# Performance work log

Measured on AMD Instinct MI355X. Metric: run time of the kernel, lower is better.

The kernel has to match this reference:

```python
import jax, jax.numpy as jnp
import numpy as np
import math

NP_, NA_ = 100000, 50000          # paper / author node counts
E0, E1, E2 = 300000, 300000, 200000  # author->paper, paper->author, paper->paper
H, D = 4, 16
HID = H * D                       # 64
IN_DIM, OUT_DIM = 128, 64
L = 2                             # num_layers
EPS = 1e-5


def _lin(x, W, b):
    return x @ W + b


def _ln(x, g, b):
    m = jnp.mean(x, axis=-1, keepdims=True)
    v = jnp.mean((x - m) ** 2, axis=-1, keepdims=True)
    return (x - m) * jax.lax.rsqrt(v + EPS) * g + b


def _segment_softmax(a, seg, n):
    m = jax.ops.segment_max(a, seg, num_segments=n)
    a = jnp.exp(a - m[seg])
    s = jax.ops.segment_sum(a, seg, num_segments=n)
    return a / (s[seg] + 1e-16)


def _hgt_conv(h_p, h_a, ei_ap, ei_pa, ei_pp,
              W_kqv, b_kqv, W_krel, W_vrel, p_rel, W_hout, b_hout, skip):
    # per-node-type fused KQV projection (HeteroDictLinear)
    kqv_p = _lin(h_p, W_kqv[0], b_kqv[0])   # [NP, 3*HID]
    kqv_a = _lin(h_a, W_kqv[1], b_kqv[1])   # [NA, 3*HID]
    k_p, q_p, v_p = [t.reshape(-1, H, D) for t in jnp.split(kqv_p, 3, axis=1)]
    k_a, q_a, v_a = [t.reshape(-1, H, D) for t in jnp.split(kqv_a, 3, axis=1)]
    # destination (query) concat order: paper then author -> dst offsets {paper:0, author:NP}
    Q = jnp.concatenate([q_p, q_a], axis=0)                    # [NP+NA, H, D]
    # per-(edge_type, head) DxD relation transforms on source k/v (k_rel / v_rel)
    # src concat order follows edge types: et0 src=author, et1 src=paper, et2 src=paper
    Ks = jnp.concatenate([
        jnp.einsum('nhd,hde->nhe', k_a, W_krel[0]),
        jnp.einsum('nhd,hde->nhe', k_p, W_krel[1]),
        jnp.einsum('nhd,hde->nhe', k_p, W_krel[2]),
    ], axis=0)                                                 # [NA+2*NP, H, D]
    Vs = jnp.concatenate([
        jnp.einsum('nhd,hde->nhe', v_a, W_vrel[0]),
        jnp.einsum('nhd,hde->nhe', v_p, W_vrel[1]),
        jnp.einsum('nhd,hde->nhe', v_p, W_vrel[2]),
    ], axis=0)
    # bipartite global edge index (src offsets: 0, NA, NA+NP; dst offsets: paper 0, author NP)
    src = jnp.concatenate([ei_ap[0], ei_pa[0] + NA_, ei_pp[0] + NA_ + NP_])
    dst = jnp.concatenate([ei_ap[1], ei_pa[1] + NP_, ei_pp[1]])
    p = jnp.concatenate([
        jnp.broadcast_to(p_rel[0], (E0, H)),
        jnp.broadcast_to(p_rel[1], (E1, H)),
        jnp.broadcast_to(p_rel[2], (E2, H)),
    ], axis=0)                                                 # [E, H]
    # edge-wise attention: alpha = (q_i * k_j).sum(-1) * p_rel / sqrt(D), segment-softmax over dst
    alpha = jnp.einsum('ehd,ehd->eh', Q[dst], Ks[src]) * p / math.sqrt(D)
    alpha = _segment_softmax(alpha, dst, NP_ + NA_)
    out = jax.ops.segment_sum(Vs[src] * alpha[:, :, None], dst,
                              num_segments=NP_ + NA_)          # [NP+NA, H, D]
    out = out.reshape(-1, HID)
    g = jax.nn.gelu(out, approximate=False)
    o_p = _lin(g[:NP_], W_hout[0], b_hout[0])
    o_a = _lin(g[NP_:], W_hout[1], b_hout[1])
    a_p = jax.nn.sigmoid(skip[0])
    a_a = jax.nn.sigmoid(skip[1])
    return a_p * o_p + (1.0 - a_p) * h_p, a_a * o_a + (1.0 - a_a) * h_a


def _forward(x_paper, x_author, ei_ap, ei_pa, ei_pp,
             W_in, b_in, W_kqv, b_kqv, W_krel, W_vrel, p_rel,
             W_hout, b_hout, skip, ln_g, ln_b, W_out, b_out):
    h_p = _lin(x_paper, W_in[0], b_in[0])
    h_a = _lin(x_author, W_in[1], b_in[1])
    for l in range(L):
        h_p, h_a = _hgt_conv(h_p, h_a, ei_ap, ei_pa, ei_pp,
                             W_kqv[l], b_kqv[l], W_krel[l], W_vrel[l],
                             p_rel[l], W_hout[l], b_hout[l], skip[l])
        h_p = jax.nn.gelu(_ln(h_p, ln_g[l, 0], ln_b[l, 0]), approximate=False)
        h_a = jax.nn.gelu(_ln(h_a, ln_g[l, 1], ln_b[l, 1]), approximate=False)
        # dropout is identity at eval
    out_p = _lin(h_p, W_out[0], b_out[0])
    out_a = _lin(h_a, W_out[1], b_out[1])
    return jnp.concatenate([out_p, out_a], axis=0)  # [NP+NA, OUT_DIM]


def setup_inputs() -> dict:
    key = jax.random.key(0)
    ks = jax.random.split(key, 20)
    f32 = jnp.float32

    def nrm(k, shape, fan_in):
        return jax.random.normal(k, shape, dtype=f32) * (1.0 / math.sqrt(fan_in))

    inp = {}
    inp['x_paper'] = jax.random.normal(ks[0], (NP_, IN_DIM), dtype=f32)
    inp['x_author'] = jax.random.normal(ks[1], (NA_, IN_DIM), dtype=f32)
    inp['ei_ap'] = jnp.stack([jax.random.randint(ks[2], (E0,), 0, NA_),
                              jax.random.randint(ks[3], (E0,), 0, NP_)]).astype(jnp.int32)
    inp['ei_pa'] = jnp.stack([jax.random.randint(ks[4], (E1,), 0, NP_),
                              jax.random.randint(ks[5], (E1,), 0, NA_)]).astype(jnp.int32)
    inp['ei_pp'] = jnp.stack([jax.random.randint(ks[6], (E2,), 0, NP_),
                              jax.random.randint(ks[7], (E2,), 0, NP_)]).astype(jnp.int32)
    inp['W_in'] = nrm(ks[8], (2, IN_DIM, HID), IN_DIM)
    inp['b_in'] = jnp.zeros((2, HID), f32)
    inp['W_kqv'] = nrm(ks[9], (L, 2, HID, 3 * HID), HID)
    inp['b_kqv'] = jnp.zeros((L, 2, 3 * HID), f32)
    inp['W_krel'] = nrm(ks[10], (L, 3, H, D, D), D)
    inp['W_vrel'] = nrm(ks[11], (L, 3, H, D, D), D)
    inp['p_rel'] = jnp.ones((L, 3, H), f32)
    inp['W_hout'] = nrm(ks[12], (L, 2, HID, HID), HID)
    inp['b_hout'] = jnp.zeros((L, 2, HID), f32)
    inp['skip'] = jnp.ones((L, 2), f32)
    inp['ln_g'] = jnp.ones((L, 2, HID), f32)
    inp['ln_b'] = jnp.zeros((L, 2, HID), f32)
    inp['W_out'] = nrm(ks[13], (2, HID, OUT_DIM), HID)
    inp['b_out'] = jnp.zeros((2, OUT_DIM), f32)
    return inp


def reference(x_paper, x_author, ei_ap, ei_pa, ei_pp,
              W_in, b_in, W_kqv, b_kqv, W_krel, W_vrel, p_rel,
              W_hout, b_hout, skip, ln_g, ln_b, W_out, b_out):
    return _forward(x_paper, x_author, ei_ap, ei_pa, ei_pp,
                    W_in, b_in, W_kqv, b_kqv, W_krel, W_vrel, p_rel,
                    W_hout, b_hout, skip, ln_g, ln_b, W_out, b_out)
```

## Files before the change

kernel.cpp:

```cpp
#include <hip/hip_runtime.h>
#include <hip/hip_bf16.h>

#define NP 100000
#define NA 50000
#define NTOT 150000
#define E0 300000
#define E1 300000
#define E2 200000
#define ETOT 800000
#define NH 4
#define HD 16
#define HID 64
#define IN_DIM 128
#define KQV 192
#define LAYERS 2
#define NSRC 250000
#define JP 320
#define JA 192
#define NCH 586
#define PT 1563
#define AT 782
#define LSPAN 33280

typedef __attribute__((ext_vector_type(8))) short bf16x8;
typedef __attribute__((ext_vector_type(4))) float f32x4;
typedef _Float16 h16x2 __attribute__((ext_vector_type(2)));

__device__ __forceinline__ float gelu_exact(float x) {
    return 0.5f * x * (1.0f + erff(x * 0.7071067811865475f));
}
__device__ __forceinline__ unsigned short f2bf(float f) {
    unsigned u = __float_as_uint(f);
    return (unsigned short)((u + 0x7fffu + ((u >> 16) & 1u)) >> 16);
}
__device__ __forceinline__ float bf2f(unsigned short b) {
    return __uint_as_float((unsigned)b << 16);
}
__device__ __forceinline__ unsigned short f2h(float f) {
    union { _Float16 h; unsigned short u; } c;
    c.h = (_Float16)f;
    return c.u;
}

__device__ __forceinline__ void edge_decode(int e, const int* __restrict__ ei_ap,
                                            const int* __restrict__ ei_pa,
                                            const int* __restrict__ ei_pp,
                                            int& src, int& dst) {
    if (e < E0)            { src = ei_ap[e];                 dst = ei_ap[E0 + e]; }
    else if (e < E0 + E1)  { int le = e - E0;
                             src = NA + ei_pa[le];           dst = NP + ei_pa[E1 + le]; }
    else                   { int le = e - E0 - E1;
                             src = NA + NP + ei_pp[le];      dst = ei_pp[E2 + le]; }
}

__global__ void csr_count_kernel(const int* __restrict__ ei_ap, const int* __restrict__ ei_pa,
                                 const int* __restrict__ ei_pp, int* __restrict__ cnt) {
    int e = blockIdx.x * 256 + threadIdx.x;
    if (e >= ETOT) return;
    int src, dst; edge_decode(e, ei_ap, ei_pa, ei_pp, src, dst);
    atomicAdd(&cnt[dst], 1);
}

__global__ void scan_chunk_sums(const int* __restrict__ cnt, int* __restrict__ csum) {
    __shared__ int sd[256];
    int c = blockIdx.x, t = threadIdx.x;
    int i = c * 256 + t;
    sd[t] = (i < NTOT) ? cnt[i] : 0;
    __syncthreads();
    for (int o = 128; o > 0; o >>= 1) { if (t < o) sd[t] += sd[t + o]; __syncthreads(); }
    if (t == 0) csum[c] = sd[0];
}

__global__ void scan_offsets(const int* __restrict__ csum, int* __restrict__ coff, int nch) {
    __shared__ int sd[1024];
    int t = threadIdx.x;
    int v = (t < nch) ? csum[t] : 0;
    sd[t] = v;
    __syncthreads();
    for (int o = 1; o < 1024; o <<= 1) {
        int x = (t >= o) ? sd[t - o] : 0;
        __syncthreads();
        sd[t] += x;
        __syncthreads();
    }
    if (t < nch) coff[t] = sd[t] - v;
}

__global__ void scan_final(const int* __restrict__ cnt, const int* __restrict__ coff,
                           int* __restrict__ row_ptr, int* __restrict__ cursor) {
    __shared__ int sd[256];
    int c = blockIdx.x, t = threadIdx.x, i = c * 256 + t;
    int v = (i < NTOT) ? cnt[i] : 0;
    sd[t] = v;
    __syncthreads();
    for (int o = 1; o < 256; o <<= 1) {
        int x = (t >= o) ? sd[t - o] : 0;
        __syncthreads();
        sd[t] += x;
        __syncthreads();
    }
    if (i < NTOT) { int ex = coff[c] + sd[t] - v; row_ptr[i] = ex; cursor[i] = ex; }
    if (i == 0) row_ptr[NTOT] = ETOT;
}

__global__ void csr_fill_kernel(const int* __restrict__ ei_ap, const int* __restrict__ ei_pa,
                                const int* __restrict__ ei_pp, int* __restrict__ cursor,
                                int* __restrict__ edge_src) {
    int e = blockIdx.x * 256 + threadIdx.x;
    if (e >= ETOT) return;
    int src, dst; edge_decode(e, ei_ap, ei_pa, ei_pp, src, dst);
    int pos = atomicAdd(&cursor[dst], 1);
    edge_src[pos] = src;
}

__global__ void prep_weights(const float* __restrict__ W_in, const float* __restrict__ W_hout,
                             const float* __restrict__ W_out,
                             unsigned short* __restrict__ WinT,
                             unsigned short* __restrict__ WhoutT,
                             unsigned short* __restrict__ WoutT) {
    int idx = blockIdx.x * 256 + threadIdx.x;
    if (idx < 2 * 64 * IN_DIM) {
        int t = idx >> 13, r = idx & 8191;
        int c = r >> 7, k = r & 127;
        WinT[idx] = f2bf(W_in[(size_t)t * IN_DIM * HID + (size_t)k * HID + c]);
        return;
    }
    int i2 = idx - 2 * 64 * IN_DIM;
    if (i2 < LAYERS * 2 * 4096) {
        int p = i2 >> 12, r = i2 & 4095;
        int c = r >> 6, k = r & 63;
        WhoutT[i2] = f2bf(W_hout[(size_t)p * 4096 + (size_t)k * HID + c]);
        return;
    }
    int i3 = i2 - LAYERS * 2 * 4096;
    if (i3 < 2 * 4096) {
        int p = i3 >> 12, r = i3 & 4095;
        int c = r >> 6, k = r & 63;
        WoutT[i3] = f2bf(W_out[(size_t)p * 4096 + (size_t)k * HID + c]);
    }
}

__global__ void fuse_weights_all(const float* __restrict__ Wkqv, const float* __restrict__ bkqv,
                                 const float* __restrict__ Wkrel, const float* __restrict__ Wvrel,
                                 unsigned short* __restrict__ WfpT, float* __restrict__ bfp,
                                 unsigned short* __restrict__ WfaT, float* __restrict__ bfa) {
    int gidx = blockIdx.x * 256 + threadIdx.x;
    if (gidx >= LAYERS * LSPAN) return;
    int lay = gidx / LSPAN;
    int idx = gidx - lay * LSPAN;
    const float* Wkqv_l = Wkqv + (size_t)lay * 2 * HID * KQV;
    const float* bkqv_l = bkqv + (size_t)lay * 2 * KQV;
    const float* Wkrel_l = Wkrel + (size_t)lay * 3 * NH * HD * HD;
    const float* Wvrel_l = Wvrel + (size_t)lay * 3 * NH * HD * HD;
    unsigned short* WfpT_l = WfpT + (size_t)lay * JP * 64;
    unsigned short* WfaT_l = WfaT + (size_t)lay * JA * 64;
    float* bfp_l = bfp + (size_t)lay * JP;
    float* bfa_l = bfa + (size_t)lay * JA;

    int type, i, j;
    if (idx < 65 * JP) { type = 0; i = idx / JP; j = idx % JP; }
    else {
        int r = idx - 65 * JP;
        type = 1; i = r / JA; j = r % JA;
    }
    int c = j >> 6, jj = j & 63, h = jj >> 4, e = jj & 15;
    const float* Wk = Wkqv_l + (size_t)type * HID * KQV;
    const float* bk = bkqv_l + type * KQV;
    float val;
    if (c == 0) {
        val = (i < 64) ? Wk[i * KQV + 64 + jj] : bk[64 + jj];
    } else {
        int et, isV;
        if (type == 0) { et = (c == 1 || c == 3) ? 1 : 2; isV = (c >= 3); }
        else           { et = 0; isV = (c == 2); }
        const float* Wr = (isV ? Wvrel_l : Wkrel_l) + (size_t)(et * NH + h) * HD * HD;
        int sb = (isV ? 128 : 0) + h * HD;
        val = 0.0f;
        #pragma unroll
        for (int d = 0; d < HD; d++) {
            float a = (i < 64) ? Wk[i * KQV + sb + d] : bk[sb + d];
            val += a * Wr[d * HD + e];
        }
    }
    if (i < 64) (type ? WfaT_l : WfpT_l)[(size_t)j * 64 + i] = f2bf(val);
    else        (type ? bfa_l : bfp_l)[j] = val;
}

__device__ __forceinline__ void mfma64(const unsigned short* A, const unsigned short* W,
                                       int wr, int wc, int lrow, int lgrp,
                                       f32x4& a00, f32x4& a01, f32x4& a10, f32x4& a11) {
    a00 = (f32x4){0.f,0.f,0.f,0.f}; a01 = a00; a10 = a00; a11 = a00;
    #pragma unroll
    for (int ks = 0; ks < 2; ks++) {
        int ko = ks * 32 + lgrp * 8;
        bf16x8 x0 = *(const bf16x8*)&A[(wr + lrow) * 72 + ko];
        bf16x8 x1 = *(const bf16x8*)&A[(wr + 16 + lrow) * 72 + ko];
        bf16x8 w0 = *(const bf16x8*)&W[(wc + lrow) * 72 + ko];
        bf16x8 w1 = *(const bf16x8*)&W[(wc + 16 + lrow) * 72 + ko];
        a00 = __builtin_amdgcn_mfma_f32_16x16x32_bf16(x0, w0, a00, 0, 0, 0);
        a01 = __builtin_amdgcn_mfma_f32_16x16x32_bf16(x0, w1, a01, 0, 0, 0);
        a10 = __builtin_amdgcn_mfma_f32_16x16x32_bf16(x1, w0, a10, 0, 0, 0);
        a11 = __builtin_amdgcn_mfma_f32_16x16x32_bf16(x1, w1, a11, 0, 0, 0);
    }
}

__device__ __forceinline__ void store_q(f32x4 a00, f32x4 a01, f32x4 a10, f32x4 a11,
                                        float bq0, float bq1, int c0, int c1, bool even,
                                        int nb, int N, int wr, int lgrp,
                                        unsigned short* Qbase) {
    #pragma unroll
    for (int mi = 0; mi < 2; mi++) {
        const f32x4 a0 = mi ? a10 : a00;
        const f32x4 a1 = mi ? a11 : a01;
        int rbase = wr + mi * 16 + lgrp * 4;
        #pragma unroll
        for (int r = 0; r < 4; r++) {
            int n = nb + rbase + r;
            unsigned own = (unsigned)f2h(a0[r] + bq0) | ((unsigned)f2h(a1[r] + bq1) << 16);
            unsigned oth = __shfl_xor(own, 1, 64);
            if (even && n < N) {
                unsigned* qp = (unsigned*)(Qbase + (size_t)n * HID);
                qp[c0 >> 1] = (own & 0xffffu) | (oth << 16);
                qp[c1 >> 1] = (own >> 16) | (oth & 0xffff0000u);
            }
        }
    }
}

__device__ __forceinline__ void store_kv(f32x4 k00, f32x4 k01, f32x4 k10, f32x4 k11,
                                         f32x4 v00, f32x4 v01, f32x4 v10, f32x4 v11,
                                         float bk0, float bk1, float bv0, float bv1,
                                         int c0, int c1, bool even,
                                         int nb, int N, int wr, int lgrp,
                                         int noff, unsigned* KVb) {
    #pragma unroll
    for (int mi = 0; mi < 2; mi++) {
        const f32x4 ak0 = mi ? k10 : k00;
        const f32x4 ak1 = mi ? k11 : k01;
        const f32x4 av0 = mi ? v10 : v00;
        const f32x4 av1 = mi ? v11 : v01;
        int rbase = wr + mi * 16 + lgrp * 4;
        #pragma unroll
        for (int r = 0; r < 4; r++) {
            int n = nb + rbase + r;
            unsigned own0 = (unsigned)f2h(ak0[r] + bk0) | ((unsigned)f2h(av0[r] + bv0) << 16);
            unsigned oth0 = __shfl_xor(own0, 1, 64);
            unsigned own1 = (unsigned)f2h(ak1[r] + bk1) | ((unsigned)f2h(av1[r] + bv1) << 16);
            unsigned oth1 = __shfl_xor(own1, 1, 64);
            if (n < N) {
                unsigned* dst = KVb + (((size_t)(noff + n)) << 6);
                unsigned w0 = even ? ((own0 & 0xffffu) | (oth0 << 16))
                                   : ((oth0 >> 16) | (own0 & 0xffff0000u));
                unsigned w1 = even ? ((own1 & 0xffffu) | (oth1 << 16))
                                   : ((oth1 >> 16) | (own1 & 0xffff0000u));
                dst[c0] = w0;
                dst[c1] = w1;
            }
        }
    }
}

__device__ __forceinline__ void kqv_phase(const unsigned short* HS,
                                          unsigned short* PA, unsigned short* PB,
                                          const unsigned short* WT, const float* bias2,
                                          int type, int tid, int nb, int N,
                                          int wr, int wc, int lrow, int lgrp,
                                          int c0, int c1, bool even,
                                          unsigned short* Qh, unsigned* KVb) {
    #pragma unroll
    for (int it = 0; it < 4; it++) {
        int idx = it * 256 + tid;
        int c = idx >> 4, kg = (idx & 15) * 4;
        *(ushort4*)&PA[c * 72 + kg] = *(const ushort4*)(WT + (size_t)c * 64 + kg);
    }
    __syncthreads();
    {
        f32x4 q00, q01, q10, q11;
        mfma64(HS, PA, wr, wc, lrow, lgrp, q00, q01, q10, q11);
        store_q(q00, q01, q10, q11, bias2[c0], bias2[c1], c0, c1, even,
                nb, N, wr, lgrp, Qh + (size_t)(type ? NP : 0) * HID);
    }
    __syncthreads();
    int ng = type ? 1 : 2;
    for (int g = 0; g < ng; g++) {
        int kc = type ? 64 : (g ? 128 : 64);
        int vc = type ? 128 : (g ? 256 : 192);
        int nf = type ? 0 : (g ? NA + NP : NA);
        #pragma unroll
        for (int it = 0; it < 4; it++) {
            int idx = it * 256 + tid;
            int c = idx >> 4, kg = (idx & 15) * 4;
            *(ushort4*)&PA[c * 72 + kg] = *(const ushort4*)(WT + (size_t)(kc + c) * 64 + kg);
            *(ushort4*)&PB[c * 72 + kg] = *(const ushort4*)(WT + (size_t)(vc + c) * 64 + kg);
        }
        __syncthreads();
        f32x4 k00, k01, k10, k11, v00, v01, v10, v11;
        mfma64(HS, PA, wr, wc, lrow, lgrp, k00, k01, k10, k11);
        mfma64(HS, PB, wr, wc, lrow, lgrp, v00, v01, v10, v11);
        store_kv(k00, k01, k10, k11, v00, v01, v10, v11,
                 bias2[kc + c0], bias2[kc + c1], bias2[vc + c0], bias2[vc + c1],
                 c0, c1, even, nb, N, wr, lgrp, nf, KVb);
        __syncthreads();
    }
}

__device__ __forceinline__ void mfma_r16(const unsigned short* X, const unsigned short* P,
                                         int w16, int lrow, int lgrp, f32x4* acc) {
    #pragma unroll
    for (int f = 0; f < 4; f++) acc[f] = (f32x4){0.f, 0.f, 0.f, 0.f};
    #pragma unroll
    for (int ks = 0; ks < 2; ks++) {
        int ko = ks * 32 + lgrp * 8;
        bf16x8 a = *(const bf16x8*)&X[(w16 + lrow) * 72 + ko];
        #pragma unroll
        for (int f = 0; f < 4; f++) {
            bf16x8 bb = *(const bf16x8*)&P[(f * 16 + lrow) * 72 + ko];
            acc[f] = __builtin_amdgcn_mfma_f32_16x16x32_bf16(a, bb, acc[f], 0, 0, 0);
        }
    }
}

__device__ __forceinline__ void store_q4(const f32x4* q, const float* bias,
                                         int lrow, int lgrp, int w16, int nb, int N,
                                         bool even, unsigned short* Qbase) {
    #pragma unroll
    for (int fp = 0; fp < 4; fp += 2) {
        int c0 = fp * 16 + lrow, c1 = c0 + 16;
        float b0 = bias[c0], b1 = bias[c1];
        #pragma unroll
        for (int r = 0; r < 4; r++) {
            int n = nb + w16 + lgrp * 4 + r;
            unsigned own = (unsigned)f2h(q[fp][r] + b0) | ((unsigned)f2h(q[fp + 1][r] + b1) << 16);
            unsigned oth = __shfl_xor(own, 1, 64);
            if (even && n < N) {
                unsigned* qp = (unsigned*)(Qbase + (size_t)n * HID);
                qp[c0 >> 1] = (own & 0xffffu) | (oth << 16);
                qp[c1 >> 1] = (own >> 16) | (oth & 0xffff0000u);
            }
        }
    }
}

__device__ __forceinline__ void store_kv4(const f32x4* kk, const f32x4* vv,
                                          const float* bias, int kc, int vc,
                                          int lrow, int lgrp, int w16, int nb, int N,
                                          bool even, int noff, unsigned* KVb) {
    #pragma unroll
    for (int fp = 0; fp < 4; fp += 2) {
        int c0 = fp * 16 + lrow, c1 = c0 + 16;
        float bk0 = bias[kc + c0], bk1 = bias[kc + c1];
        float bv0 = bias[vc + c0], bv1 = bias[vc + c1];
        #pragma unroll
        for (int r = 0; r < 4; r++) {
            int n = nb + w16 + lgrp * 4 + r;
            unsigned own0 = (unsigned)f2h(kk[fp][r] + bk0) | ((unsigned)f2h(vv[fp][r] + bv0) << 16);
            unsigned oth0 = __shfl_xor(own0, 1, 64);
            unsigned own1 = (unsigned)f2h(kk[fp + 1][r] + bk1) | ((unsigned)f2h(vv[fp + 1][r] + bv1) << 16);
            unsigned oth1 = __shfl_xor(own1, 1, 64);
            if (n < N) {
                unsigned* dst = KVb + (((size_t)(noff + n)) << 6);
                unsigned w0 = even ? ((own0 & 0xffffu) | (oth0 << 16))
                                   : ((oth0 >> 16) | (own0 & 0xffff0000u));
                unsigned w1 = even ? ((own1 & 0xffffu) | (oth1 << 16))
                                   : ((oth1 >> 16) | (own1 & 0xffff0000u));
                dst[c0] = w0;
                dst[c1] = w1;
            }
        }
    }
}

#define STAGE_PANEL(dst, src)                                                   \
    { _Pragma("unroll")                                                         \
      for (int it_ = 0; it_ < 4; it_++) {                                       \
          int idx_ = it_ * 256 + tid;                                           \
          int c_ = idx_ >> 4, kg_ = (idx_ & 15) * 4;                            \
          *(ushort4*)&dst[c_ * 72 + kg_] =                                      \
              *(const ushort4*)((src) + (size_t)c_ * 64 + kg_);                 \
      } }

__global__ __launch_bounds__(256) void gemm_in_kqv(
    const float* __restrict__ xp, const float* __restrict__ xa,
    const unsigned short* __restrict__ WinT, const float* __restrict__ b_in,
    const unsigned short* __restrict__ WfpT, const float* __restrict__ bfp,
    const unsigned short* __restrict__ WfaT, const float* __restrict__ bfa,
    unsigned short* __restrict__ Hb, unsigned short* __restrict__ Qh,
    unsigned* __restrict__ KVb)
{
    __shared__ unsigned short smem[17408];
    unsigned short* XB  = smem;
    unsigned short* WTl = smem + 8704;
    unsigned short* HS  = smem;
    unsigned short* PA  = smem + 4608;
    unsigned short* PB  = smem + 9216;

    int b = blockIdx.x, tid = threadIdx.x;
    int type = (b >= PT);
    int tile = type ? (b - PT) : b;
    int N = type ? NA : NP;
    const float* X = type ? xa : xp;
    const unsigned short* WT = WinT + (size_t)type * 64 * IN_DIM;
    const float* bias = b_in + type * HID;
    unsigned short* H = Hb + (type ? (size_t)NP * HID : 0);
    int nb = tile * 64;

    {
        int row = tid >> 2, cg = (tid & 3) * 32;
        int n = nb + row;
        if (n < N) {
            const float* xr = X + (size_t)n * IN_DIM + cg;
            #pragma unroll
            for (int i = 0; i < 32; i += 4) {
                float4 v = *(const float4*)(xr + i);
                *(ushort4*)&XB[row * 136 + cg + i] =
                    make_ushort4(f2bf(v.x), f2bf(v.y), f2bf(v.z), f2bf(v.w));
            }
        } else {
            #pragma unroll
            for (int i = 0; i < 32; i += 4)
                *(ushort4*)&XB[row * 136 + cg + i] = make_ushort4(0, 0, 0, 0);
        }
    }
    #pragma unroll
    for (int it = 0; it < 8; it++) {
        int idx = it * 256 + tid;
        int c = idx >> 5, kg = (idx & 31) * 4;
        *(ushort4*)&WTl[c * 136 + kg] = *(const ushort4*)(WT + (size_t)c * IN_DIM + kg);
    }
    __syncthreads();

    int w = tid >> 6, lane = tid & 63;
    int wr = (w >> 1) * 32, wc = (w & 1) * 32;
    int lrow = lane & 15, lgrp = lane >> 4;
    int c0 = wc + lrow, c1 = wc + 16 + lrow;
    bool even = ((lrow & 1) == 0);

    f32x4 acc00 = {0.f,0.f,0.f,0.f}, acc01 = {0.f,0.f,0.f,0.f};
    f32x4 acc10 = {0.f,0.f,0.f,0.f}, acc11 = {0.f,0.f,0.f,0.f};
    #pragma unroll
    for (int ks = 0; ks < 4; ks++) {
        int ko = ks * 32 + lgrp * 8;
        bf16x8 a0 = *(const bf16x8*)&XB[(wr + lrow) * 136 + ko];
        bf16x8 a1 = *(const bf16x8*)&XB[(wr + 16 + lrow) * 136 + ko];
        bf16x8 b0 = *(const bf16x8*)&WTl[(wc + lrow) * 136 + ko];
        bf16x8 b1 = *(const bf16x8*)&WTl[(wc + 16 + lrow) * 136 + ko];
        acc00 = __builtin_amdgcn_mfma_f32_16x16x32_bf16(a0, b0, acc00, 0, 0, 0);
        acc01 = __builtin_amdgcn_mfma_f32_16x16x32_bf16(a0, b1, acc01, 0, 0, 0);
        acc10 = __builtin_amdgcn_mfma_f32_16x16x32_bf16(a1, b0, acc10, 0, 0, 0);
        acc11 = __builtin_amdgcn_mfma_f32_16x16x32_bf16(a1, b1, acc11, 0, 0, 0);
    }
    __syncthreads();

    float bias0 = bias[c0], bias1 = bias[c1];
    #pragma unroll
    for (int mi = 0; mi < 2; mi++) {
        const f32x4 accn0 = mi ? acc10 : acc00;
        const f32x4 accn1 = mi ? acc11 : acc01;
        int rbase = wr + mi * 16 + lgrp * 4;
        #pragma unroll
        for (int r = 0; r < 4; r++) {
            int n = nb + rbase + r;
            unsigned short h0 = f2bf(accn0[r] + bias0);
            unsigned short h1 = f2bf(accn1[r] + bias1);
            HS[(rbase + r) * 72 + c0] = h0;
            HS[(rbase + r) * 72 + c1] = h1;
            unsigned own = (unsigned)h0 | ((unsigned)h1 << 16);
            unsigned oth = __shfl_xor(own, 1, 64);
            if (even && n < N) {
                unsigned* hp = (unsigned*)(H + (size_t)n * HID);
                hp[c0 >> 1] = (own & 0xffffu) | (oth << 16);
                hp[c1 >> 1] = (own >> 16) | (oth & 0xffff0000u);
            }
        }
    }
    __syncthreads();

    const unsigned short* WT2 = type ? WfaT : WfpT;
    const float* bias2 = type ? bfa : bfp;
    kqv_phase(HS, PA, PB, WT2, bias2, type, tid, nb, N,
              wr, wc, lrow, lgrp, c0, c1, even, Qh, KVb);
}

__global__ __launch_bounds__(256) void attn_kernel(
    const unsigned short* __restrict__ Qh, const unsigned* __restrict__ KVb,
    const float* __restrict__ p_rel, const int* __restrict__ row_ptr,
    const int* __restrict__ edge_src, unsigned short* __restrict__ ABf)
{
    int wid = threadIdx.x >> 6, lane = threadIdx.x & 63;
    int n = blockIdx.x * 4 + wid;
    if (n >= NTOT) return;
    int half = lane >> 5;
    int p = lane & 31;
    int h = p >> 3;
    unsigned qw = *(const unsigned*)(Qh + (((size_t)n) << 6) + 2 * p);
    union { unsigned u; h16x2 v; _Float16 f[2]; } qc; qc.u = qw;
    h16x2 qh = qc.v;
    const float INV_LN2 = 1.4426950408889634f;
    float pr0 = p_rel[h] * 0.25f * INV_LN2;
    float pr1 = p_rel[4 + h] * 0.25f * INV_LN2;
    float pr2 = p_rel[8 + h] * 0.25f * INV_LN2;
    int beg = row_ptr[n], end = row_ptr[n + 1];
    float s = 0.0f, acc0 = 0.f, acc1 = 0.f;
    for (int e = beg; e < end; e += 4) {
        int e0 = e + half;
        int e1 = e + 2 + half;
        bool v0 = (e0 < end), v1 = (e1 < end);
        int s0 = v0 ? edge_src[e0] : 0;
        int s1 = v1 ? edge_src[e1] : 0;
        uint2 kv0 = *(const uint2*)(KVb + (((size_t)s0) << 6) + 2 * p);
        uint2 kv1 = *(const uint2*)(KVb + (((size_t)s1) << 6) + 2 * p);
        float d0, d1;
#if __has_builtin(__builtin_amdgcn_fdot2)
        {
            union { unsigned u; h16x2 v; } ck;
            ck.u = kv0.x; d0 = __builtin_amdgcn_fdot2(qh, ck.v, 0.0f, false);
            ck.u = kv1.x; d1 = __builtin_amdgcn_fdot2(qh, ck.v, 0.0f, false);
        }
#else
        {
            union { unsigned u; _Float16 f[2]; } ck;
            float q0 = (float)qc.f[0], q1 = (float)qc.f[1];
            ck.u = kv0.x; d0 = q0 * (float)ck.f[0] + q1 * (float)ck.f[1];
            ck.u = kv1.x; d1 = q0 * (float)ck.f[0] + q1 * (float)ck.f[1];
        }
#endif
        d0 += __shfl_xor(d0, 1, 64);  d1 += __shfl_xor(d1, 1, 64);
        d0 += __shfl_xor(d0, 2, 64);  d1 += __shfl_xor(d1, 2, 64);
        d0 += __shfl_xor(d0, 4, 64);  d1 += __shfl_xor(d1, 4, 64);
        float pa = (s0 < NA) ? pr0 : ((s0 < NA + NP) ? pr1 : pr2);
        float pb = (s1 < NA) ? pr0 : ((s1 < NA + NP) ? pr1 : pr2);
        float a0 = v0 ? fminf(d0 * pa, 80.0f) : -INFINITY;
        float a1 = v1 ? fminf(d1 * pb, 80.0f) : -INFINITY;
        float p0 = exp2f(a0);
        float p1 = exp2f(a1);
        s += p0 + p1;
        union { unsigned u; _Float16 f[2]; } cv0, cv1;
        cv0.u = kv0.y; cv1.u = kv1.y;
        acc0 += p0 * (float)cv0.f[0] + p1 * (float)cv1.f[0];
        acc1 += p0 * (float)cv0.f[1] + p1 * (float)cv1.f[1];
    }
    s    += __shfl_xor(s, 32, 64);
    acc0 += __shfl_xor(acc0, 32, 64);
    acc1 += __shfl_xor(acc1, 32, 64);
    if (half == 0) {
        float inv = 1.0f / (s + 1e-16f);
        unsigned pack = (unsigned)f2bf(acc0 * inv) | ((unsigned)f2bf(acc1 * inv) << 16);
        *(unsigned*)(ABf + (((size_t)n) << 6) + 2 * p) = pack;
    }
}

__global__ __launch_bounds__(256) void gemm_hout_fused(
    const unsigned short* __restrict__ ABf, const unsigned short* __restrict__ WhT,
    const float* __restrict__ bhout, const float* __restrict__ skip_p,
    const float* __restrict__ lng, const float* __restrict__ lnb,
    unsigned short* __restrict__ Hb,
    const unsigned short* __restrict__ WfpT, const float* __restrict__ bfp,
    const unsigned short* __restrict__ WfaT, const float* __restrict__ bfa,
    unsigned short* __restrict__ Qh, unsigned* __restrict__ KVb,
    const unsigned short* __restrict__ WoT, const float* __restrict__ bout,
    float* __restrict__ outp)
{
    __shared__ unsigned short smem[13824];
    unsigned short* XbS = smem;
    unsigned short* PA  = smem + 4608;
    unsigned short* PB  = smem + 9216;

    int b = blockIdx.x, tid = threadIdx.x;
    int type = (b >= PT);
    int tile = type ? (b - PT) : b;
    int N = type ? NA : NP;
    size_t base_off = type ? (size_t)NP * HID : 0;
    const unsigned short* X = ABf + base_off;
    const unsigned short* W = WhT + (size_t)type * 4096;
    const float* bias = bhout + type * HID;
    unsigned short* H = Hb + base_off;
    int nb = tile * 64;
    bool fin = (WoT != nullptr);

    {
        int row = tid >> 2, cg = (tid & 3) * 16;
        int n = nb + row;
        unsigned short tmp[16];
        if (n < N) {
            const unsigned short* xr = X + (((size_t)n) << 6) + cg;
            #pragma unroll
            for (int i = 0; i < 16; i += 4) {
                ushort4 v = *(const ushort4*)(xr + i);
                tmp[i]   = f2bf(gelu_exact(bf2f(v.x)));
                tmp[i+1] = f2bf(gelu_exact(bf2f(v.y)));
                tmp[i+2] = f2bf(gelu_exact(bf2f(v.z)));
                tmp[i+3] = f2bf(gelu_exact(bf2f(v.w)));
            }
        } else {
            #pragma unroll
            for (int i = 0; i < 16; i++) tmp[i] = 0;
        }
        #pragma unroll
        for (int i = 0; i < 16; i += 4)
            *(ushort4*)&XbS[row * 72 + cg + i] =
                make_ushort4(tmp[i], tmp[i+1], tmp[i+2], tmp[i+3]);
    }
    STAGE_PANEL(PA, W)
    __syncthreads();

    int w = tid >> 6, lane = tid & 63;
    int lrow = lane & 15, lgrp = lane >> 4;
    int w16 = w * 16;
    bool even = ((lrow & 1) == 0);

    f32x4 acc[4];
    mfma_r16(XbS, PA, w16, lrow, lgrp, acc);
    const unsigned short* WT2 = type ? WfaT : WfpT;
    const float* bias2 = type ? bfa : bfp;
    STAGE_PANEL(PB, fin ? (WoT + (size_t)type * 4096) : WT2)

    float a = 1.0f / (1.0f + __expf(-skip_p[type]));
    float oma = 1.0f - a;
    float lnv[4][4];
    {
        float bh[4], gg[4], ll[4];
        #pragma unroll
        for (int f = 0; f < 4; f++) {
            int c = f * 16 + lrow;
            bh[f] = bias[c];
            gg[f] = lng[type * HID + c];
            ll[f] = lnb[type * HID + c];
        }
        #pragma unroll
        for (int r = 0; r < 4; r++) {
            int n = nb + w16 + lgrp * 4 + r;
            float x0, x1, x2, x3;
            if (n < N) {
                const unsigned short* hp = H + (size_t)n * HID;
                x0 = a * (acc[0][r] + bh[0]) + oma * bf2f(hp[0 * 16 + lrow]);
                x1 = a * (acc[1][r] + bh[1]) + oma * bf2f(hp[1 * 16 + lrow]);
                x2 = a * (acc[2][r] + bh[2]) + oma * bf2f(hp[2 * 16 + lrow]);
                x3 = a * (acc[3][r] + bh[3]) + oma * bf2f(hp[3 * 16 + lrow]);
            } else { x0 = x1 = x2 = x3 = 0.f; }
            float sum = x0 + x1 + x2 + x3;
            sum += __shfl_xor(sum, 1, 64); sum += __shfl_xor(sum, 2, 64);
            sum += __shfl_xor(sum, 4, 64); sum += __shfl_xor(sum, 8, 64);
            float mean = sum * (1.0f / 64.0f);
            float d0 = x0 - mean, d1 = x1 - mean, d2 = x2 - mean, d3 = x3 - mean;
            float sq = d0*d0 + d1*d1 + d2*d2 + d3*d3;
            sq += __shfl_xor(sq, 1, 64); sq += __shfl_xor(sq, 2, 64);
            sq += __shfl_xor(sq, 4, 64); sq += __shfl_xor(sq, 8, 64);
            float rstd = rsqrtf(sq * (1.0f / 64.0f) + 1e-5f);
            lnv[r][0] = gelu_exact(d0 * rstd * gg[0] + ll[0]);
            lnv[r][1] = gelu_exact(d1 * rstd * gg[1] + ll[1]);
            lnv[r][2] = gelu_exact(d2 * rstd * gg[2] + ll[2]);
            lnv[r][3] = gelu_exact(d3 * rstd * gg[3] + ll[3]);
            if (!fin && n < N) {
                #pragma unroll
                for (int fp = 0; fp < 4; fp += 2) {
                    int c0 = fp * 16 + lrow, c1 = c0 + 16;
                    unsigned own = (unsigned)f2bf(lnv[r][fp]) | ((unsigned)f2bf(lnv[r][fp + 1]) << 16);
                    unsigned oth = __shfl_xor(own, 1, 64);
                    if (even) {
                        unsigned* hp2 = (unsigned*)(H + (size_t)n * HID);
                        hp2[c0 >> 1] = (own & 0xffffu) | (oth << 16);
                        hp2[c1 >> 1] = (own >> 16) | (oth & 0xffff0000u);
                    }
                }
            } else if (!fin) {
                #pragma unroll
                for (int fp = 0; fp < 4; fp += 2) {
                    unsigned own = 0;
                    (void)__shfl_xor(own, 1, 64);
                }
            }
        }
    }
    __syncthreads();

    #pragma unroll
    for (int r = 0; r < 4; r++) {
        int row = w16 + lgrp * 4 + r;
        #pragma unroll
        for (int f = 0; f < 4; f++)
            XbS[row * 72 + f * 16 + lrow] = f2bf(lnv[r][f]);
    }
    __syncthreads();

    if (fin) {
        f32x4 o[4];
        mfma_r16(XbS, PB, w16, lrow, lgrp, o);
        const float* b2 = bout + type * HID;
        float* O = outp + base_off;
        #pragma unroll
        for (int f = 0; f < 4; f++) {
            int c = f * 16 + lrow;
            float bb = b2[c];
            #pragma unroll
            for (int r = 0; r < 4; r++) {
                int n = nb + w16 + lgrp * 4 + r;
                if (n < N) O[(size_t)n * HID + c] = o[f][r] + bb;
            }
        }
        return;
    }

    int kc1 = 64, vc1 = type ? 128 : 192;
    int nf1 = type ? 0 : NA;
    {
        f32x4 q[4];
        mfma_r16(XbS, PB, w16, lrow, lgrp, q);
        STAGE_PANEL(PA, WT2 + (size_t)kc1 * 64)
        store_q4(q, bias2, lrow, lgrp, w16, nb, N, even,
                 Qh + (size_t)(type ? NP : 0) * HID);
    }
    __syncthreads();

    f32x4 kk[4];
    mfma_r16(XbS, PA, w16, lrow, lgrp, kk);
    STAGE_PANEL(PB, WT2 + (size_t)vc1 * 64)
    __syncthreads();

    {
        f32x4 vv[4];
        mfma_r16(XbS, PB, w16, lrow, lgrp, vv);
        if (type == 0) STAGE_PANEL(PA, WT2 + (size_t)128 * 64)
        store_kv4(kk, vv, bias2, kc1, vc1, lrow, lgrp, w16, nb, N, even, nf1, KVb);
    }
    if (type == 0) {
        __syncthreads();
        mfma_r16(XbS, PA, w16, lrow, lgrp, kk);
        STAGE_PANEL(PB, WT2 + (size_t)256 * 64)
        __syncthreads();
        f32x4 vv[4];
        mfma_r16(XbS, PB, w16, lrow, lgrp, vv);
        store_kv4(kk, vv, bias2, 128, 256, lrow, lgrp, w16, nb, N, even, NA + NP, KVb);
    }
}

extern "C" void kernel_launch(void* const* d_in, const int* in_sizes, int n_in,
                              void* d_out, int out_size, void* d_ws, size_t ws_size,
                              hipStream_t stream) {
    const float* x_paper  = (const float*)d_in[0];
    const float* x_author = (const float*)d_in[1];
    const int*   ei_ap    = (const int*)d_in[2];
    const int*   ei_pa    = (const int*)d_in[3];
    const int*   ei_pp    = (const int*)d_in[4];
    const float* W_in     = (const float*)d_in[5];
    const float* b_in     = (const float*)d_in[6];
    const float* W_kqv    = (const float*)d_in[7];
    const float* b_kqv    = (const float*)d_in[8];
    const float* W_krel   = (const float*)d_in[9];
    const float* W_vrel   = (const float*)d_in[10];
    const float* p_rel    = (const float*)d_in[11];
    const float* W_hout   = (const float*)d_in[12];
    const float* b_hout   = (const float*)d_in[13];
    const float* skip     = (const float*)d_in[14];
    const float* ln_g     = (const float*)d_in[15];
    const float* ln_b     = (const float*)d_in[16];
    const float* W_out    = (const float*)d_in[17];
    const float* b_out    = (const float*)d_in[18];
    float* out            = (float*)d_out;

    char* ws = (char*)d_ws;
    unsigned short* Hb  = (unsigned short*)ws;
    unsigned short* Qh  = Hb + (size_t)NTOT * HID;
    unsigned* KVb       = (unsigned*)(Qh + (size_t)NTOT * HID);
    unsigned short* ABf = (unsigned short*)(KVb + (size_t)NSRC * HID);
    unsigned short* WfpT = ABf + (size_t)NTOT * HID;
    float* bfp  = (float*)(WfpT + (size_t)2 * JP * 64);
    unsigned short* WfaT = (unsigned short*)(bfp + 2 * JP);
    float* bfa  = (float*)(WfaT + (size_t)2 * JA * 64);
    unsigned short* WinT   = (unsigned short*)(bfa + 2 * JA);
    unsigned short* WhoutT = WinT + 2 * 64 * IN_DIM;
    unsigned short* WoutT  = WhoutT + LAYERS * 2 * 64 * 64;
    int* cnt      = (int*)(WoutT + 2 * 64 * 64);
    int* row_ptr  = cnt + NTOT;
    int* cursor   = row_ptr + NTOT + 16;
    int* edge_src = cursor + NTOT;
    int* csum     = edge_src + ETOT;
    int* coff     = csum + 1024;

    dim3 blk(256);
    const int EB = (ETOT + 255) / 256;

    hipMemsetAsync(cnt, 0, NTOT * sizeof(int), stream);
    csr_count_kernel<<<EB, blk, 0, stream>>>(ei_ap, ei_pa, ei_pp, cnt);
    scan_chunk_sums<<<NCH, blk, 0, stream>>>(cnt, csum);
    scan_offsets<<<1, 1024, 0, stream>>>(csum, coff, NCH);
    scan_final<<<NCH, blk, 0, stream>>>(cnt, coff, row_ptr, cursor);
    csr_fill_kernel<<<EB, blk, 0, stream>>>(ei_ap, ei_pa, ei_pp, cursor, edge_src);

    prep_weights<<<(2*64*IN_DIM + LAYERS*2*4096 + 2*4096 + 255) / 256, blk, 0, stream>>>(
        W_in, W_hout, W_out, WinT, WhoutT, WoutT);
    fuse_weights_all<<<(LAYERS * LSPAN + 255) / 256, blk, 0, stream>>>(
        W_kqv, b_kqv, W_krel, W_vrel, WfpT, bfp, WfaT, bfa);

    gemm_in_kqv<<<PT + AT, blk, 0, stream>>>(
        x_paper, x_author, WinT, b_in,
        WfpT, bfp, WfaT, bfa, Hb, Qh, KVb);
    attn_kernel<<<(NTOT + 3) / 4, blk, 0, stream>>>(
        Qh, KVb, p_rel, row_ptr, edge_src, ABf);
    gemm_hout_fused<<<PT + AT, blk, 0, stream>>>(
        ABf, WhoutT, b_hout, skip, ln_g, ln_b, Hb,
        WfpT + (size_t)JP * 64, bfp + JP, WfaT + (size_t)JA * 64, bfa + JA,
        Qh, KVb, nullptr, nullptr, nullptr);
    attn_kernel<<<(NTOT + 3) / 4, blk, 0, stream>>>(
        Qh, KVb, p_rel + 3 * NH, row_ptr, edge_src, ABf);
    gemm_hout_fused<<<PT + AT, blk, 0, stream>>>(
        ABf, WhoutT + (size_t)2 * 4096, b_hout + 2 * HID, skip + 2,
        ln_g + 2 * HID, ln_b + 2 * HID, Hb,
        nullptr, nullptr, nullptr, nullptr, Qh, KVb,
        WoutT, b_out, out);
}
```

Before: 342.9 us.

## Read MFMA weight fragments directly from global memory instead of staging in LDS

Weight panels for the input, KQV and output GEMMs are no longer copied into shared memory. Each wave loads its B fragments straight from global memory, where they should be cache-resident. Each wave now owns a 16-row slab of the tile, so X staging and compute become wave-local, and most __syncthreads barriers and the LDS footprint go away, which could raise occupancy. The cost is repeated global/L2 fragment loads per wave and uncoalesced 16-byte reads.

```diff
diff --git a/kernel.cpp b/kernel.cpp
--- a/kernel.cpp
+++ b/kernel.cpp
@@ -186,135 +186,37 @@
     else        (type ? bfa_l : bfp_l)[j] = val;
 }
 
-__device__ __forceinline__ void mfma64(const unsigned short* A, const unsigned short* W,
-                                       int wr, int wc, int lrow, int lgrp,
-                                       f32x4& a00, f32x4& a01, f32x4& a10, f32x4& a11) {
-    a00 = (f32x4){0.f,0.f,0.f,0.f}; a01 = a00; a10 = a00; a11 = a00;
+__device__ __forceinline__ void mfma_r16g(const unsigned short* __restrict__ X,
+                                          const unsigned short* __restrict__ Wg,
+                                          int w16, int lrow, int lgrp, f32x4* acc) {
+    bf16x8 bfr[4][2];
+    #pragma unroll
+    for (int f = 0; f < 4; f++)
+        #pragma unroll
+        for (int ks = 0; ks < 2; ks++)
+            bfr[f][ks] = *(const bf16x8*)(Wg + (size_t)(f * 16 + lrow) * 64 + ks * 32 + lgrp * 8);
+    #pragma unroll
+    for (int f = 0; f < 4; f++) acc[f] = (f32x4){0.f, 0.f, 0.f, 0.f};
     #pragma unroll
     for (int ks = 0; ks < 2; ks++) {
-        int ko = ks * 32 + lgrp * 8;
-        bf16x8 x0 = *(const bf16x8*)&A[(wr + lrow) * 72 + ko];
-        bf16x8 x1 = *(const bf16x8*)&A[(wr + 16 + lrow) * 72 + ko];
-        bf16x8 w0 = *(const bf16x8*)&W[(wc + lrow) * 72 + ko];
-        bf16x8 w1 = *(const bf16x8*)&W[(wc + 16 + lrow) * 72 + ko];
-        a00 = __builtin_amdgcn_mfma_f32_16x16x32_bf16(x0, w0, a00, 0, 0, 0);
-        a01 = __builtin_amdgcn_mfma_f32_16x16x32_bf16(x0, w1, a01, 0, 0, 0);
-        a10 = __builtin_amdgcn_mfma_f32_16x16x32_bf16(x1, w0, a10, 0, 0, 0);
-        a11 = __builtin_amdgcn_mfma_f32_16x16x32_bf16(x1, w1, a11, 0, 0, 0);
-    }
-}
-
-__device__ __forceinline__ void store_q(f32x4 a00, f32x4 a01, f32x4 a10, f32x4 a11,
-                                        float bq0, float bq1, int c0, int c1, bool even,
-                                        int nb, int N, int wr, int lgrp,
-                                        unsigned short* Qbase) {
-    #pragma unroll
-    for (int mi = 0; mi < 2; mi++) {
-        const f32x4 a0 = mi ? a10 : a00;
-        const f32x4 a1 = mi ? a11 : a01;
-        int rbase = wr + mi * 16 + lgrp * 4;
-        #pragma unroll
-        for (int r = 0; r < 4; r++) {
-            int n = nb + rbase + r;
-            unsigned own = (unsigned)f2h(a0[r] + bq0) | ((unsigned)f2h(a1[r] + bq1) << 16);
-            unsigned oth = __shfl_xor(own, 1, 64);
-            if (even && n < N) {
-                unsigned* qp = (unsigned*)(Qbase + (size_t)n * HID);
-                qp[c0 >> 1] = (own & 0xffffu) | (oth << 16);
-                qp[c1 >> 1] = (own >> 16) | (oth & 0xffff0000u);
-            }
-        }
-    }
-}
-
-__device__ __forceinline__ void store_kv(f32x4 k00, f32x4 k01, f32x4 k10, f32x4 k11,
-                                         f32x4 v00, f32x4 v01, f32x4 v10, f32x4 v11,
-                                         float bk0, float bk1, float bv0, float bv1,
-                                         int c0, int c1, bool even,
-                                         int nb, int N, int wr, int lgrp,
-                                         int noff, unsigned* KVb) {
-    #pragma unroll
-    for (int mi = 0; mi < 2; mi++) {
-        const f32x4 ak0 = mi ? k10 : k00;
-        const f32x4 ak1 = mi ? k11 : k01;
-        const f32x4 av0 = mi ? v10 : v00;
-        const f32x4 av1 = mi ? v11 : v01;
-        int rbase = wr + mi * 16 + lgrp * 4;
-        #pragma unroll
-        for (int r = 0; r < 4; r++) {
-            int n = nb + rbase + r;
-            unsigned own0 = (unsigned)f2h(ak0[r] + bk0) | ((unsigned)f2h(av0[r] + bv0) << 16);
-            unsigned oth0 = __shfl_xor(own0, 1, 64);
-            unsigned own1 = (unsigned)f2h(ak1[r] + bk1) | ((unsigned)f2h(av1[r] + bv1) << 16);
-            unsigned oth1 = __shfl_xor(own1, 1, 64);
-            if (n < N) {
-                unsigned* dst = KVb + (((size_t)(noff + n)) << 6);
-                unsigned w0 = even ? ((own0 & 0xffffu) | (oth0 << 16))
-                                   : ((oth0 >> 16) | (own0 & 0xffff0000u));
-                unsigned w1 = even ? ((own1 & 0xffffu) | (oth1 << 16))
-                                   : ((oth1 >> 16) | (own1 & 0xffff0000u));
-                dst[c0] = w0;
-                dst[c1] = w1;
-            }
-        }
-    }
-}
-
-__device__ __forceinline__ void kqv_phase(const unsigned short* HS,
-                                          unsigned short* PA, unsigned short* PB,
-                                          const unsigned short* WT, const float* bias2,
-                                          int type, int tid, int nb, int N,
-                                          int wr, int wc, int lrow, int lgrp,
-                                          int c0, int c1, bool even,
-                                          unsigned short* Qh, unsigned* KVb) {
-    #pragma unroll
-    for (int it = 0; it < 4; it++) {
-        int idx = it * 256 + tid;
-        int c = idx >> 4, kg = (idx & 15) * 4;
-        *(ushort4*)&PA[c * 72 + kg] = *(const ushort4*)(WT + (size_t)c * 64 + kg);
-    }
-    __syncthreads();
-    {
-        f32x4 q00, q01, q10, q11;
-        mfma64(HS, PA, wr, wc, lrow, lgrp, q00, q01, q10, q11);
-        store_q(q00, q01, q10, q11, bias2[c0], bias2[c1], c0, c1, even,
-                nb, N, wr, lgrp, Qh + (size_t)(type ? NP : 0) * HID);
-    }
-    __syncthreads();
-    int ng = type ? 1 : 2;
-    for (int g = 0; g < ng; g++) {
-        int kc = type ? 64 : (g ? 128 : 64);
-        int vc = type ? 128 : (g ? 256 : 192);
-        int nf = type ? 0 : (g ? NA + NP : NA);
-        #pragma unroll
-        for (int it = 0; it < 4; it++) {
-            int idx = it * 256 + tid;
-            int c = idx >> 4, kg = (idx & 15) * 4;
-            *(ushort4*)&PA[c * 72 + kg] = *(const ushort4*)(WT + (size_t)(kc + c) * 64 + kg);
-            *(ushort4*)&PB[c * 72 + kg] = *(const ushort4*)(WT + (size_t)(vc + c) * 64 + kg);
-        }
-        __syncthreads();
-        f32x4 k00, k01, k10, k11, v00, v01, v10, v11;
-        mfma64(HS, PA, wr, wc, lrow, lgrp, k00, k01, k10, k11);
-        mfma64(HS, PB, wr, wc, lrow, lgrp, v00, v01, v10, v11);
-        store_kv(k00, k01, k10, k11, v00, v01, v10, v11,
-                 bias2[kc + c0], bias2[kc + c1], bias2[vc + c0], bias2[vc + c1],
-                 c0, c1, even, nb, N, wr, lgrp, nf, KVb);
-        __syncthreads();
-    }
-}
-
-__device__ __forceinline__ void mfma_r16(const unsigned short* X, const unsigned short* P,
-                                         int w16, int lrow, int lgrp, f32x4* acc) {
+        bf16x8 a = *(const bf16x8*)&X[(w16 + lrow) * 72 + ks * 32 + lgrp * 8];
+        #pragma unroll
+        for (int f = 0; f < 4; f++)
+            acc[f] = __builtin_amdgcn_mfma_f32_16x16x32_bf16(a, bfr[f][ks], acc[f], 0, 0, 0);
+    }
+}
+
+__device__ __forceinline__ void mfma_r16g_k128(const unsigned short* __restrict__ X,
+                                               const unsigned short* __restrict__ Wg,
+                                               int w16, int lrow, int lgrp, f32x4* acc) {
     #pragma unroll
     for (int f = 0; f < 4; f++) acc[f] = (f32x4){0.f, 0.f, 0.f, 0.f};
     #pragma unroll
-    for (int ks = 0; ks < 2; ks++) {
-        int ko = ks * 32 + lgrp * 8;
-        bf16x8 a = *(const bf16x8*)&X[(w16 + lrow) * 72 + ko];
+    for (int ks = 0; ks < 4; ks++) {
+        bf16x8 a = *(const bf16x8*)&X[(w16 + lrow) * 136 + ks * 32 + lgrp * 8];
         #pragma unroll
         for (int f = 0; f < 4; f++) {
-            bf16x8 bb = *(const bf16x8*)&P[(f * 16 + lrow) * 72 + ko];
+            bf16x8 bb = *(const bf16x8*)(Wg + (size_t)(f * 16 + lrow) * 128 + ks * 32 + lgrp * 8);
             acc[f] = __builtin_amdgcn_mfma_f32_16x16x32_bf16(a, bb, acc[f], 0, 0, 0);
         }
     }
@@ -370,14 +272,28 @@
     }
 }
 
-#define STAGE_PANEL(dst, src)                                                   \
-    { _Pragma("unroll")                                                         \
-      for (int it_ = 0; it_ < 4; it_++) {                                       \
-          int idx_ = it_ * 256 + tid;                                           \
-          int c_ = idx_ >> 4, kg_ = (idx_ & 15) * 4;                            \
-          *(ushort4*)&dst[c_ * 72 + kg_] =                                      \
-              *(const ushort4*)((src) + (size_t)c_ * 64 + kg_);                 \
-      } }
+__device__ __forceinline__ void kqv_tail_g(const unsigned short* __restrict__ XS,
+                                           const unsigned short* __restrict__ WT2,
+                                           const float* __restrict__ bias2,
+                                           int type, int nb, int N,
+                                           int w16, int lrow, int lgrp, bool even,
+                                           unsigned short* __restrict__ Qh,
+                                           unsigned* __restrict__ KVb) {
+    f32x4 q[4];
+    mfma_r16g(XS, WT2, w16, lrow, lgrp, q);
+    store_q4(q, bias2, lrow, lgrp, w16, nb, N, even, Qh + (size_t)(type ? NP : 0) * HID);
+    int kc1 = 64, vc1 = type ? 128 : 192;
+    int nf1 = type ? 0 : NA;
+    f32x4 kk[4], vv[4];
+    mfma_r16g(XS, WT2 + (size_t)kc1 * 64, w16, lrow, lgrp, kk);
+    mfma_r16g(XS, WT2 + (size_t)vc1 * 64, w16, lrow, lgrp, vv);
+    store_kv4(kk, vv, bias2, kc1, vc1, lrow, lgrp, w16, nb, N, even, nf1, KVb);
+    if (type == 0) {
+        mfma_r16g(XS, WT2 + (size_t)128 * 64, w16, lrow, lgrp, kk);
+        mfma_r16g(XS, WT2 + (size_t)256 * 64, w16, lrow, lgrp, vv);
+        store_kv4(kk, vv, bias2, 128, 256, lrow, lgrp, w16, nb, N, even, NA + NP, KVb);
+    }
+}
 
 __global__ __launch_bounds__(256) void gemm_in_kqv(
     const float* __restrict__ xp, const float* __restrict__ xa,
@@ -387,12 +303,8 @@
     unsigned short* __restrict__ Hb, unsigned short* __restrict__ Qh,
     unsigned* __restrict__ KVb)
 {
-    __shared__ unsigned short smem[17408];
-    unsigned short* XB  = smem;
-    unsigned short* WTl = smem + 8704;
-    unsigned short* HS  = smem;
-    unsigned short* PA  = smem + 4608;
-    unsigned short* PB  = smem + 9216;
+    __shared__ unsigned short XB[64 * 136];
+    __shared__ unsigned short HS[64 * 72];
 
     int b = blockIdx.x, tid = threadIdx.x;
     int type = (b >= PT);
@@ -404,8 +316,12 @@
     unsigned short* H = Hb + (type ? (size_t)NP * HID : 0);
     int nb = tile * 64;
 
+    int w = tid >> 6, lane = tid & 63;
+    int w16 = w * 16, lrow = lane & 15, lgrp = lane >> 4;
+    bool even = ((lrow & 1) == 0);
+
     {
-        int row = tid >> 2, cg = (tid & 3) * 32;
+        int row = w16 + (lane >> 2), cg = (lane & 3) * 32;
         int n = nb + row;
         if (n < N) {
             const float* xr = X + (size_t)n * IN_DIM + cg;
@@ -421,50 +337,27 @@
                 *(ushort4*)&XB[row * 136 + cg + i] = make_ushort4(0, 0, 0, 0);
         }
     }
-    #pragma unroll
-    for (int it = 0; it < 8; it++) {
-        int idx = it * 256 + tid;
-        int c = idx >> 5, kg = (idx & 31) * 4;
-        *(ushort4*)&WTl[c * 136 + kg] = *(const ushort4*)(WT + (size_t)c * IN_DIM + kg);
-    }
     __syncthreads();
 
-    int w = tid >> 6, lane = tid & 63;
-    int wr = (w >> 1) * 32, wc = (w & 1) * 32;
-    int lrow = lane & 15, lgrp = lane >> 4;
-    int c0 = wc + lrow, c1 = wc + 16 + lrow;
-    bool even = ((lrow & 1) == 0);
-
-    f32x4 acc00 = {0.f,0.f,0.f,0.f}, acc01 = {0.f,0.f,0.f,0.f};
-    f32x4 acc10 = {0.f,0.f,0.f,0.f}, acc11 = {0.f,0.f,0.f,0.f};
-    #pragma unroll
-    for (int ks = 0; ks < 4; ks++) {
-        int ko = ks * 32 + lgrp * 8;
-        bf16x8 a0 = *(const bf16x8*)&XB[(wr + lrow) * 136 + ko];
-        bf16x8 a1 = *(const bf16x8*)&XB[(wr + 16 + lrow) * 136 + ko];
-        bf16x8 b0 = *(const bf16x8*)&WTl[(wc + lrow) * 136 + ko];
-        bf16x8 b1 = *(const bf16x8*)&WTl[(wc + 16 + lrow) * 136 + ko];
-        acc00 = __builtin_amdgcn_mfma_f32_16x16x32_bf16(a0, b0, acc00, 0, 0, 0);
-        acc01 = __builtin_amdgcn_mfma_f32_16x16x32_bf16(a0, b1, acc01, 0, 0, 0);
-        acc10 = __builtin_amdgcn_mfma_f32_16x16x32_bf16(a1, b0, acc10, 0, 0, 0);
-        acc11 = __builtin_amdgcn_mfma_f32_16x16x32_bf16(a1, b1, acc11, 0, 0, 0);
-    }
-    __syncthreads();
-
-    float bias0 = bias[c0], bias1 = bias[c1];
-    #pragma unroll
-    for (int mi = 0; mi < 2; mi++) {
-        const f32x4 accn0 = mi ? acc10 : acc00;
-        const f32x4 accn1 = mi ? acc11 : acc01;
-        int rbase = wr + mi * 16 + lgrp * 4;
-        #pragma unroll
-        for (int r = 0; r < 4; r++) {
-            int n = nb + rbase + r;
-            unsigned short h0 = f2bf(accn0[r] + bias0);
-            unsigned short h1 = f2bf(accn1[r] + bias1);
-            HS[(rbase + r) * 72 + c0] = h0;
-            HS[(rbase + r) * 72 + c1] = h1;
-            unsigned own = (unsigned)h0 | ((unsigned)h1 << 16);
+    f32x4 acc[4];
+    mfma_r16g_k128(XB, WT, w16, lrow, lgrp, acc);
+
+    float bh[4];
+    #pragma unroll
+    for (int f = 0; f < 4; f++) bh[f] = bias[f * 16 + lrow];
+    #pragma unroll
+    for (int r = 0; r < 4; r++) {
+        int n = nb + w16 + lgrp * 4 + r;
+        float hv[4];
+        #pragma unroll
+        for (int f = 0; f < 4; f++) {
+            hv[f] = acc[f][r] + bh[f];
+            HS[(w16 + lgrp * 4 + r) * 72 + f * 16 + lrow] = f2bf(hv[f]);
+        }
+        #pragma unroll
+        for (int fp = 0; fp < 4; fp += 2) {
+            int c0 = fp * 16 + lrow, c1 = c0 + 16;
+            unsigned own = (unsigned)f2bf(hv[fp]) | ((unsigned)f2bf(hv[fp + 1]) << 16);
             unsigned oth = __shfl_xor(own, 1, 64);
             if (even && n < N) {
                 unsigned* hp = (unsigned*)(H + (size_t)n * HID);
@@ -477,8 +370,7 @@
 
     const unsigned short* WT2 = type ? WfaT : WfpT;
     const float* bias2 = type ? bfa : bfp;
-    kqv_phase(HS, PA, PB, WT2, bias2, type, tid, nb, N,
-              wr, wc, lrow, lgrp, c0, c1, even, Qh, KVb);
+    kqv_tail_g(HS, WT2, bias2, type, nb, N, w16, lrow, lgrp, even, Qh, KVb);
 }
 
 __global__ __launch_bounds__(256) void attn_kernel(
@@ -560,10 +452,7 @@
     const unsigned short* __restrict__ WoT, const float* __restrict__ bout,
     float* __restrict__ outp)
 {
-    __shared__ unsigned short smem[13824];
-    unsigned short* XbS = smem;
-    unsigned short* PA  = smem + 4608;
-    unsigned short* PB  = smem + 9216;
+    __shared__ unsigned short XbS[64 * 72];
 
     int b = blockIdx.x, tid = threadIdx.x;
     int type = (b >= PT);
@@ -577,8 +466,12 @@
     int nb = tile * 64;
     bool fin = (WoT != nullptr);
 
+    int w = tid >> 6, lane = tid & 63;
+    int w16 = w * 16, lrow = lane & 15, lgrp = lane >> 4;
+    bool even = ((lrow & 1) == 0);
+
     {
-        int row = tid >> 2, cg = (tid & 3) * 16;
+        int row = w16 + (lane >> 2), cg = (lane & 3) * 16;
         int n = nb + row;
         unsigned short tmp[16];
         if (n < N) {
@@ -600,19 +493,10 @@
             *(ushort4*)&XbS[row * 72 + cg + i] =
                 make_ushort4(tmp[i], tmp[i+1], tmp[i+2], tmp[i+3]);
     }
-    STAGE_PANEL(PA, W)
     __syncthreads();
 
-    int w = tid >> 6, lane = tid & 63;
-    int lrow = lane & 15, lgrp = lane >> 4;
-    int w16 = w * 16;
-    bool even = ((lrow & 1) == 0);
-
     f32x4 acc[4];
-    mfma_r16(XbS, PA, w16, lrow, lgrp, acc);
-    const unsigned short* WT2 = type ? WfaT : WfpT;
-    const float* bias2 = type ? bfa : bfp;
-    STAGE_PANEL(PB, fin ? (WoT + (size_t)type * 4096) : WT2)
+    mfma_r16g(XbS, W, w16, lrow, lgrp, acc);
 
     float a = 1.0f / (1.0f + __expf(-skip_p[type]));
     float oma = 1.0f - a;
@@ -650,28 +534,21 @@
             lnv[r][1] = gelu_exact(d1 * rstd * gg[1] + ll[1]);
             lnv[r][2] = gelu_exact(d2 * rstd * gg[2] + ll[2]);
             lnv[r][3] = gelu_exact(d3 * rstd * gg[3] + ll[3]);
-            if (!fin && n < N) {
+            if (!fin) {
                 #pragma unroll
                 for (int fp = 0; fp < 4; fp += 2) {
                     int c0 = fp * 16 + lrow, c1 = c0 + 16;
                     unsigned own = (unsigned)f2bf(lnv[r][fp]) | ((unsigned)f2bf(lnv[r][fp + 1]) << 16);
                     unsigned oth = __shfl_xor(own, 1, 64);
-                    if (even) {
+                    if (even && n < N) {
                         unsigned* hp2 = (unsigned*)(H + (size_t)n * HID);
                         hp2[c0 >> 1] = (own & 0xffffu) | (oth << 16);
                         hp2[c1 >> 1] = (own >> 16) | (oth & 0xffff0000u);
                     }
                 }
-            } else if (!fin) {
-                #pragma unroll
-                for (int fp = 0; fp < 4; fp += 2) {
-                    unsigned own = 0;
-                    (void)__shfl_xor(own, 1, 64);
-                }
             }
         }
     }
-    __syncthreads();
 
     #pragma unroll
     for (int r = 0; r < 4; r++) {
@@ -684,7 +561,7 @@
 
     if (fin) {
         f32x4 o[4];
-        mfma_r16(XbS, PB, w16, lrow, lgrp, o);
+        mfma_r16g(XbS, WoT + (size_t)type * 4096, w16, lrow, lgrp, o);
         const float* b2 = bout + type * HID;
         float* O = outp + base_off;
         #pragma unroll
@@ -697,39 +574,10 @@
                 if (n < N) O[(size_t)n * HID + c] = o[f][r] + bb;
             }
         }
-        return;
-    }
-
-    int kc1 = 64, vc1 = type ? 128 : 192;
-    int nf1 = type ? 0 : NA;
-    {
-        f32x4 q[4];
-        mfma_r16(XbS, PB, w16, lrow, lgrp, q);
-        STAGE_PANEL(PA, WT2 + (size_t)kc1 * 64)
-        store_q4(q, bias2, lrow, lgrp, w16, nb, N, even,
-                 Qh + (size_t)(type ? NP : 0) * HID);
-    }
-    __syncthreads();
-
-    f32x4 kk[4];
-    mfma_r16(XbS, PA, w16, lrow, lgrp, kk);
-    STAGE_PANEL(PB, WT2 + (size_t)vc1 * 64)
-    __syncthreads();
-
-    {
-        f32x4 vv[4];
-        mfma_r16(XbS, PB, w16, lrow, lgrp, vv);
-        if (type == 0) STAGE_PANEL(PA, WT2 + (size_t)128 * 64)
-        store_kv4(kk, vv, bias2, kc1, vc1, lrow, lgrp, w16, nb, N, even, nf1, KVb);
-    }
-    if (type == 0) {
-        __syncthreads();
-        mfma_r16(XbS, PA, w16, lrow, lgrp, kk);
-        STAGE_PANEL(PB, WT2 + (size_t)256 * 64)
-        __syncthreads();
-        f32x4 vv[4];
-        mfma_r16(XbS, PB, w16, lrow, lgrp, vv);
-        store_kv4(kk, vv, bias2, 128, 256, lrow, lgrp, w16, nb, N, even, NA + NP, KVb);
+    } else {
+        const unsigned short* WT2 = type ? WfaT : WfpT;
+        const float* bias2 = type ? bfa : bfp;
+        kqv_tail_g(XbS, WT2, bias2, type, nb, N, w16, lrow, lgrp, even, Qh, KVb);
     }
 }
 
```

Result: slower. 419.9 us (+22.5%).
